# Optimization experiments

Hardware: AMD Instinct MI355X
Metric: run time of the kernel (lower is better)

## Reference

```python
import jax, jax.numpy as jnp
import numpy as np

MAX_DIST = 50.0
NO_NEIGHBORS = 0.0
# feature order: [dx, dy, size_a, size_b, angle]; angle mark is cyclic
FEATURES_RANGE = np.array([50.0, 50.0, 32.0, 32.0, np.pi], dtype=np.float32)
FEATURES_CYCLIC = np.array([False, False, False, False, True])


def setup_inputs() -> dict:
    key = jax.random.key(0)
    ks = jax.random.split(key, 8)
    B, N, M, F, H = 8, 1024, 1024, 5, 4
    points = jax.random.normal(ks[0], (B, N, F), jnp.float32)
    context_points = jax.random.normal(ks[1], (B, M, F), jnp.float32)
    points_mask = jnp.ones((B, N), dtype=bool)
    context_points_mask = jnp.ones((B, M), dtype=bool)
    distance_matrix = jax.random.uniform(ks[2], (B, N, M), jnp.float32) * 100.0
    interactions_mask = jax.random.randint(ks[3], (B, N, M), 0, 2).astype(bool)
    # q_fun MLP: Linear(5,4) -> ReLU -> Linear(4,1) -> Sigmoid
    W1 = jax.random.normal(ks[4], (F, H), jnp.float32) / np.sqrt(F)
    b1 = jnp.zeros((H,), jnp.float32)
    W2 = jax.random.normal(ks[5], (H, 1), jnp.float32) / np.sqrt(H)
    b2 = jnp.zeros((1,), jnp.float32)
    # attention weight model: Linear(5,1)
    Wa = jax.random.normal(ks[6], (F, 1), jnp.float32) / np.sqrt(F)
    ba = jnp.zeros((1,), jnp.float32)
    return dict(points=points, points_mask=points_mask,
                context_points=context_points, context_points_mask=context_points_mask,
                distance_matrix=distance_matrix, interactions_mask=interactions_mask,
                global_max_dist=100,
                W1=W1, b1=b1, W2=W2, b2=b2, Wa=Wa, ba=ba)


def reference(points, points_mask, context_points, context_points_mask,
              distance_matrix, interactions_mask, global_max_dist,
              W1, b1, W2, b2, Wa, ba):
    fr = jnp.asarray(FEATURES_RANGE)
    cyc = jnp.asarray(FEATURES_CYCLIC)
    # pairwise abs feature differences: [B, N, M, 5]
    fd = jnp.abs(points[:, :, None, :] - context_points[:, None, :, :])
    fn = fd / fr
    fc = jnp.remainder(fn, 1.0)
    fc = jnp.minimum(fc, 1.0 - fc)           # cyclic wrap-around distance
    fn = jnp.where(cyc, fc, fn)
    # q_fun MLP + sigmoid -> per-pair similarity energy [B, N, M]
    h = jax.nn.relu(jnp.einsum('bnmf,fh->bnmh', fn, W1) + b1)
    energy = jax.nn.sigmoid(jnp.einsum('bnmh,ho->bnmo', h, W2) + b2)[..., 0]
    # interaction mask, tightened by max_dist when max_dist < global_max_dist
    ib = interactions_mask
    if MAX_DIST < global_max_dist:
        ib = ib & (distance_matrix <= MAX_DIST)
    # masked attention reduce over context axis (dim 2)
    scores = (jnp.einsum('bnmf,fo->bnmo', fn, Wa) + ba)[..., 0]
    scores = jnp.where(ib, scores, -jnp.inf)
    weights = jax.nn.softmax(scores, axis=2)  # all-masked rows -> NaN
    reduced = jnp.sum(weights * energy, axis=2)
    reduced = jnp.nan_to_num(reduced, nan=NO_NEIGHBORS,
                             posinf=NO_NEIGHBORS, neginf=NO_NEIGHBORS)
    return reduced
```

## Files before the change

### kernel.cpp

```cpp
#include <hip/hip_runtime.h>
#include <math.h>

#define BATCH   8
#define NPTS    1024
#define MCTX    1024
#define BN      (BATCH * NPTS)

#define INV_R0  0.02f
#define INV_R1  0.02f
#define INV_R2  0.03125f
#define INV_R3  0.03125f
#define INV_PI  0.3183098861837907f
#define MAX_DIST 50.0f
#define LOG2E   1.4426950408889634f

__global__ __launch_bounds__(512) void sim_kernel(
    const float* __restrict__ points,
    const float* __restrict__ ctx,
    const float* __restrict__ dist,
    const unsigned char* __restrict__ imask,
    const int* __restrict__ gmd_p,
    const float* __restrict__ W1p,
    const float* __restrict__ b1p,
    const float* __restrict__ W2p,
    const float* __restrict__ b2p,
    const float* __restrict__ Wap,
    const float* __restrict__ bap,
    float* __restrict__ out)
{
    __shared__ float4         sA[MCTX];
    __shared__ float          s4[MCTX];
    __shared__ unsigned short q[8][MCTX];

    const int wid  = threadIdx.x >> 6;
    const int lane = threadIdx.x & 63;
    const int row  = blockIdx.x * 8 + wid;
    const int b    = row >> 10;

    const float* __restrict__ cb = ctx + (size_t)b * MCTX * 5;
    const int m0 = threadIdx.x, m1 = threadIdx.x + 512;
    const float r00 = cb[m0*5+0], r01 = cb[m0*5+1], r02 = cb[m0*5+2],
                r03 = cb[m0*5+3], r04 = cb[m0*5+4];
    const float r10 = cb[m1*5+0], r11 = cb[m1*5+1], r12 = cb[m1*5+2],
                r13 = cb[m1*5+3], r14 = cb[m1*5+4];

    const float4*       __restrict__ d4  = (const float4*)(dist + (size_t)row * MCTX);
    const unsigned int* __restrict__ m4p = (const unsigned int*)(imask + (size_t)row * MCTX);
    float4 dv0 = d4[lane],       dv1 = d4[lane + 64],
           dv2 = d4[lane + 128], dv3 = d4[lane + 192];
    unsigned int mv0 = m4p[lane],       mv1 = m4p[lane + 64],
                 mv2 = m4p[lane + 128], mv3 = m4p[lane + 192];

    sA[m0] = make_float4(r00, r01, r02, r03);
    s4[m0] = r04 * INV_PI;
    sA[m1] = make_float4(r10, r11, r12, r13);
    s4[m1] = r14 * INV_PI;
    __syncthreads();

    const float ir[4] = { INV_R0, INV_R1, INV_R2, INV_R3 };
    float w1s[20];
#pragma unroll
    for (int f = 0; f < 5; ++f) {
        const float s = (f < 4) ? ir[f] : 1.0f;
#pragma unroll
        for (int j = 0; j < 4; ++j) w1s[f*4+j] = W1p[f*4+j] * s;
    }
    float b1v[4];
#pragma unroll
    for (int j = 0; j < 4; ++j) b1v[j] = b1p[j];
    float w2n[4];
#pragma unroll
    for (int j = 0; j < 4; ++j) w2n[j] = W2p[j] * (-LOG2E);
    const float b2n = b2p[0] * (-LOG2E);
    float wan[5];
#pragma unroll
    for (int f = 0; f < 5; ++f) wan[f] = Wap[f] * LOG2E * ((f < 4) ? ir[f] : 1.0f);
    const float ban = bap[0] * LOG2E;

    const float p0 = points[row*5+0], p1 = points[row*5+1], p2 = points[row*5+2],
                p3 = points[row*5+3], p4s = points[row*5+4] * INV_PI;

    const bool tighten = (MAX_DIST < (float)gmd_p[0]);

    unsigned okbits = 0;
    {
        const float4 dvv[4] = { dv0, dv1, dv2, dv3 };
        const unsigned int mvv[4] = { mv0, mv1, mv2, mv3 };
#pragma unroll
        for (int j = 0; j < 4; ++j) {
            const float dd[4] = { dvv[j].x, dvv[j].y, dvv[j].z, dvv[j].w };
#pragma unroll
            for (int t = 0; t < 4; ++t) {
                bool ok = ((mvv[j] >> (8*t)) & 0xFFu) != 0u;
                if (tighten) ok = ok && (dd[t] <= MAX_DIST);
                okbits |= ok ? (1u << (4*j + t)) : 0u;
            }
        }
    }

    int tot = 0;
#pragma unroll
    for (int k = 0; k < 16; ++k) {
        const bool ok = (okbits >> k) & 1u;
        unsigned long long bm = __ballot(ok);
        unsigned rank = __builtin_amdgcn_mbcnt_hi(
                            (unsigned)(bm >> 32),
                            __builtin_amdgcn_mbcnt_lo((unsigned)bm, 0u));
        if (ok) {
            const int m = (lane + 64 * (k >> 2)) * 4 + (k & 3);
            q[wid][tot + rank] = (unsigned short)m;
        }
        tot += (int)__popcll(bm);
    }

    float lsum = 0.0f, asum = 0.0f;
#pragma unroll 2
    for (int i = lane; i < tot; i += 64) {
        const int m = (int)q[wid][i];
        const float4 cA  = sA[m];
        const float  c4v = s4[m];

        const float a0 = fabsf(p0 - cA.x);
        const float a1 = fabsf(p1 - cA.y);
        const float a2 = fabsf(p2 - cA.z);
        const float a3 = fabsf(p3 - cA.w);
        float g   = __builtin_amdgcn_fractf(fabsf(p4s - c4v));
        float fn4 = fminf(g, 1.0f - g);

        float h0 = fmaxf(0.0f, b1v[0] + a0*w1s[0] + a1*w1s[4] + a2*w1s[8]  + a3*w1s[12] + fn4*w1s[16]);
        float h1 = fmaxf(0.0f, b1v[1] + a0*w1s[1] + a1*w1s[5] + a2*w1s[9]  + a3*w1s[13] + fn4*w1s[17]);
        float h2 = fmaxf(0.0f, b1v[2] + a0*w1s[2] + a1*w1s[6] + a2*w1s[10] + a3*w1s[14] + fn4*w1s[18]);
        float h3 = fmaxf(0.0f, b1v[3] + a0*w1s[3] + a1*w1s[7] + a2*w1s[11] + a3*w1s[15] + fn4*w1s[19]);

        float zn = b2n + h0*w2n[0] + h1*w2n[1] + h2*w2n[2] + h3*w2n[3];
        float energy = __builtin_amdgcn_rcpf(1.0f + __builtin_amdgcn_exp2f(zn));

        float sc = ban + a0*wan[0] + a1*wan[1] + a2*wan[2] + a3*wan[3] + fn4*wan[4];
        float e  = __builtin_amdgcn_exp2f(sc);

        lsum += e;
        asum = fmaf(e, energy, asum);
    }

#pragma unroll
    for (int off = 1; off < 64; off <<= 1) {
        lsum += __shfl_xor(lsum, off, 64);
        asum += __shfl_xor(asum, off, 64);
    }

    if (lane == 0) {
        out[row] = (lsum > 0.0f) ? (asum / lsum) : 0.0f;
    }
}

extern "C" void kernel_launch(void* const* d_in, const int* in_sizes, int n_in,
                              void* d_out, int out_size, void* d_ws, size_t ws_size,
                              hipStream_t stream) {
    const float*         points = (const float*)d_in[0];
    const float*         ctx    = (const float*)d_in[2];
    const float*         dist   = (const float*)d_in[4];
    const unsigned char* imask  = (const unsigned char*)d_in[5];
    const int*           gmd    = (const int*)d_in[6];
    const float*         W1     = (const float*)d_in[7];
    const float*         b1     = (const float*)d_in[8];
    const float*         W2     = (const float*)d_in[9];
    const float*         b2     = (const float*)d_in[10];
    const float*         Wa     = (const float*)d_in[11];
    const float*         ba     = (const float*)d_in[12];
    float*               out    = (float*)d_out;

    dim3 block(512);
    dim3 grid(BN / 8);
    sim_kernel<<<grid, block, 0, stream>>>(points, ctx, dist, imask, gmd,
                                           W1, b1, W2, b2, Wa, ba, out);
}
```

Measured before the change: 15.47 us.

## Process two rows per wave to amortize context staging across more rows

Each block now handles 16 rows, two per wave, halving the grid so the per-block load of the batch's context points into shared memory and the weight setup are shared by twice as many rows. The second row's distance and mask loads are issued after the barrier so they can overlap with the first row's compaction and compute. The cost is fewer blocks (512 instead of 1024) on a 256-CU device, higher register pressure from holding the second row's loads, and serialized per-wave work. The shared queue is reused across the two rows within each wave.

```diff
diff --git a/kernel.cpp b/kernel.cpp
--- a/kernel.cpp
+++ b/kernel.cpp
@@ -13,6 +13,78 @@
 #define INV_PI  0.3183098861837907f
 #define MAX_DIST 50.0f
 #define LOG2E   1.4426950408889634f
+
+#define PROC_ROW(DV0, DV1, DV2, DV3, MV0, MV1, MV2, MV3, P0, P1, P2, P3, P4S, ROW)   \
+  do {                                                                               \
+    unsigned okbits = 0;                                                             \
+    {                                                                                \
+      const float dd0[4] = { DV0.x, DV0.y, DV0.z, DV0.w };                           \
+      const float dd1[4] = { DV1.x, DV1.y, DV1.z, DV1.w };                           \
+      const float dd2[4] = { DV2.x, DV2.y, DV2.z, DV2.w };                           \
+      const float dd3[4] = { DV3.x, DV3.y, DV3.z, DV3.w };                           \
+      _Pragma("unroll")                                                              \
+      for (int t = 0; t < 4; ++t) {                                                  \
+        bool ok0 = ((MV0 >> (8*t)) & 0xFFu) != 0u;                                   \
+        bool ok1 = ((MV1 >> (8*t)) & 0xFFu) != 0u;                                   \
+        bool ok2 = ((MV2 >> (8*t)) & 0xFFu) != 0u;                                   \
+        bool ok3 = ((MV3 >> (8*t)) & 0xFFu) != 0u;                                   \
+        if (tighten) {                                                               \
+          ok0 = ok0 && (dd0[t] <= MAX_DIST);                                         \
+          ok1 = ok1 && (dd1[t] <= MAX_DIST);                                         \
+          ok2 = ok2 && (dd2[t] <= MAX_DIST);                                         \
+          ok3 = ok3 && (dd3[t] <= MAX_DIST);                                         \
+        }                                                                            \
+        okbits |= ok0 ? (1u << (0  + t)) : 0u;                                       \
+        okbits |= ok1 ? (1u << (4  + t)) : 0u;                                       \
+        okbits |= ok2 ? (1u << (8  + t)) : 0u;                                       \
+        okbits |= ok3 ? (1u << (12 + t)) : 0u;                                       \
+      }                                                                              \
+    }                                                                                \
+    int tot = 0;                                                                     \
+    _Pragma("unroll")                                                                \
+    for (int k = 0; k < 16; ++k) {                                                   \
+      const bool ok = (okbits >> k) & 1u;                                            \
+      unsigned long long bm = __ballot(ok);                                          \
+      unsigned rank = __builtin_amdgcn_mbcnt_hi(                                     \
+                          (unsigned)(bm >> 32),                                      \
+                          __builtin_amdgcn_mbcnt_lo((unsigned)bm, 0u));              \
+      if (ok) {                                                                      \
+        const int m = (lane + 64 * (k >> 2)) * 4 + (k & 3);                          \
+        q[wid][tot + rank] = (unsigned short)m;                                      \
+      }                                                                              \
+      tot += (int)__popcll(bm);                                                      \
+    }                                                                                \
+    float lsum = 0.0f, asum = 0.0f;                                                  \
+    _Pragma("unroll 2")                                                              \
+    for (int i = lane; i < tot; i += 64) {                                           \
+      const int m = (int)q[wid][i];                                                  \
+      const float4 cA  = sA[m];                                                      \
+      const float  c4v = s4[m];                                                      \
+      const float a0 = fabsf(P0 - cA.x);                                             \
+      const float a1 = fabsf(P1 - cA.y);                                             \
+      const float a2 = fabsf(P2 - cA.z);                                             \
+      const float a3 = fabsf(P3 - cA.w);                                             \
+      float g   = __builtin_amdgcn_fractf(fabsf(P4S - c4v));                         \
+      float fn4 = fminf(g, 1.0f - g);                                                \
+      float h0 = fmaxf(0.0f, b1v[0] + a0*w1s[0] + a1*w1s[4] + a2*w1s[8]  + a3*w1s[12] + fn4*w1s[16]); \
+      float h1 = fmaxf(0.0f, b1v[1] + a0*w1s[1] + a1*w1s[5] + a2*w1s[9]  + a3*w1s[13] + fn4*w1s[17]); \
+      float h2 = fmaxf(0.0f, b1v[2] + a0*w1s[2] + a1*w1s[6] + a2*w1s[10] + a3*w1s[14] + fn4*w1s[18]); \
+      float h3 = fmaxf(0.0f, b1v[3] + a0*w1s[3] + a1*w1s[7] + a2*w1s[11] + a3*w1s[15] + fn4*w1s[19]); \
+      float zn = b2n + h0*w2n[0] + h1*w2n[1] + h2*w2n[2] + h3*w2n[3];                \
+      float energy = __builtin_amdgcn_rcpf(1.0f + __builtin_amdgcn_exp2f(zn));       \
+      float sc = ban + a0*wan[0] + a1*wan[1] + a2*wan[2] + a3*wan[3] + fn4*wan[4];   \
+      float e  = __builtin_amdgcn_exp2f(sc);                                         \
+      lsum += e;                                                                     \
+      asum = fmaf(e, energy, asum);                                                  \
+    }                                                                                \
+    _Pragma("unroll")                                                                \
+    for (int off = 1; off < 64; off <<= 1) {                                         \
+      lsum += __shfl_xor(lsum, off, 64);                                             \
+      asum += __shfl_xor(asum, off, 64);                                             \
+    }                                                                                \
+    if (lane == 0)                                                                   \
+      out[ROW] = (lsum > 0.0f) ? (asum / lsum) : 0.0f;                               \
+  } while (0)
 
 __global__ __launch_bounds__(512) void sim_kernel(
     const float* __restrict__ points,
@@ -34,8 +106,10 @@
 
     const int wid  = threadIdx.x >> 6;
     const int lane = threadIdx.x & 63;
-    const int row  = blockIdx.x * 8 + wid;
-    const int b    = row >> 10;
+    const int rb   = blockIdx.x * 16;
+    const int b    = rb >> 10;
+    const int row0 = rb + wid * 2;
+    const int row1 = row0 + 1;
 
     const float* __restrict__ cb = ctx + (size_t)b * MCTX * 5;
     const int m0 = threadIdx.x, m1 = threadIdx.x + 512;
@@ -44,18 +118,25 @@
     const float r10 = cb[m1*5+0], r11 = cb[m1*5+1], r12 = cb[m1*5+2],
                 r13 = cb[m1*5+3], r14 = cb[m1*5+4];
 
-    const float4*       __restrict__ d4  = (const float4*)(dist + (size_t)row * MCTX);
-    const unsigned int* __restrict__ m4p = (const unsigned int*)(imask + (size_t)row * MCTX);
-    float4 dv0 = d4[lane],       dv1 = d4[lane + 64],
-           dv2 = d4[lane + 128], dv3 = d4[lane + 192];
-    unsigned int mv0 = m4p[lane],       mv1 = m4p[lane + 64],
-                 mv2 = m4p[lane + 128], mv3 = m4p[lane + 192];
+    const float4*       __restrict__ dA = (const float4*)(dist + (size_t)row0 * MCTX);
+    const unsigned int* __restrict__ mA = (const unsigned int*)(imask + (size_t)row0 * MCTX);
+    const float4 Adv0 = dA[lane],       Adv1 = dA[lane + 64],
+                 Adv2 = dA[lane + 128], Adv3 = dA[lane + 192];
+    const unsigned int Amv0 = mA[lane],       Amv1 = mA[lane + 64],
+                       Amv2 = mA[lane + 128], Amv3 = mA[lane + 192];
 
     sA[m0] = make_float4(r00, r01, r02, r03);
     s4[m0] = r04 * INV_PI;
     sA[m1] = make_float4(r10, r11, r12, r13);
     s4[m1] = r14 * INV_PI;
     __syncthreads();
+
+    const float4*       __restrict__ dB = (const float4*)(dist + (size_t)row1 * MCTX);
+    const unsigned int* __restrict__ mB = (const unsigned int*)(imask + (size_t)row1 * MCTX);
+    const float4 Bdv0 = dB[lane],       Bdv1 = dB[lane + 64],
+                 Bdv2 = dB[lane + 128], Bdv3 = dB[lane + 192];
+    const unsigned int Bmv0 = mB[lane],       Bmv1 = mB[lane + 64],
+                       Bmv2 = mB[lane + 128], Bmv3 = mB[lane + 192];
 
     const float ir[4] = { INV_R0, INV_R1, INV_R2, INV_R3 };
     float w1s[20];
@@ -77,80 +158,17 @@
     for (int f = 0; f < 5; ++f) wan[f] = Wap[f] * LOG2E * ((f < 4) ? ir[f] : 1.0f);
     const float ban = bap[0] * LOG2E;
 
-    const float p0 = points[row*5+0], p1 = points[row*5+1], p2 = points[row*5+2],
-                p3 = points[row*5+3], p4s = points[row*5+4] * INV_PI;
+    const float p00 = points[row0*5+0], p01 = points[row0*5+1], p02 = points[row0*5+2],
+                p03 = points[row0*5+3], p04s = points[row0*5+4] * INV_PI;
+    const float p10 = points[row1*5+0], p11 = points[row1*5+1], p12 = points[row1*5+2],
+                p13 = points[row1*5+3], p14s = points[row1*5+4] * INV_PI;
 
     const bool tighten = (MAX_DIST < (float)gmd_p[0]);
 
-    unsigned okbits = 0;
-    {
-        const float4 dvv[4] = { dv0, dv1, dv2, dv3 };
-        const unsigned int mvv[4] = { mv0, mv1, mv2, mv3 };
-#pragma unroll
-        for (int j = 0; j < 4; ++j) {
-            const float dd[4] = { dvv[j].x, dvv[j].y, dvv[j].z, dvv[j].w };
-#pragma unroll
-            for (int t = 0; t < 4; ++t) {
-                bool ok = ((mvv[j] >> (8*t)) & 0xFFu) != 0u;
-                if (tighten) ok = ok && (dd[t] <= MAX_DIST);
-                okbits |= ok ? (1u << (4*j + t)) : 0u;
-            }
-        }
-    }
-
-    int tot = 0;
-#pragma unroll
-    for (int k = 0; k < 16; ++k) {
-        const bool ok = (okbits >> k) & 1u;
-        unsigned long long bm = __ballot(ok);
-        unsigned rank = __builtin_amdgcn_mbcnt_hi(
-                            (unsigned)(bm >> 32),
-                            __builtin_amdgcn_mbcnt_lo((unsigned)bm, 0u));
-        if (ok) {
-            const int m = (lane + 64 * (k >> 2)) * 4 + (k & 3);
-            q[wid][tot + rank] = (unsigned short)m;
-        }
-        tot += (int)__popcll(bm);
-    }
-
-    float lsum = 0.0f, asum = 0.0f;
-#pragma unroll 2
-    for (int i = lane; i < tot; i += 64) {
-        const int m = (int)q[wid][i];
-        const float4 cA  = sA[m];
-        const float  c4v = s4[m];
-
-        const float a0 = fabsf(p0 - cA.x);
-        const float a1 = fabsf(p1 - cA.y);
-        const float a2 = fabsf(p2 - cA.z);
-        const float a3 = fabsf(p3 - cA.w);
-        float g   = __builtin_amdgcn_fractf(fabsf(p4s - c4v));
-        float fn4 = fminf(g, 1.0f - g);
-
-        float h0 = fmaxf(0.0f, b1v[0] + a0*w1s[0] + a1*w1s[4] + a2*w1s[8]  + a3*w1s[12] + fn4*w1s[16]);
-        float h1 = fmaxf(0.0f, b1v[1] + a0*w1s[1] + a1*w1s[5] + a2*w1s[9]  + a3*w1s[13] + fn4*w1s[17]);
-        float h2 = fmaxf(0.0f, b1v[2] + a0*w1s[2] + a1*w1s[6] + a2*w1s[10] + a3*w1s[14] + fn4*w1s[18]);
-        float h3 = fmaxf(0.0f, b1v[3] + a0*w1s[3] + a1*w1s[7] + a2*w1s[11] + a3*w1s[15] + fn4*w1s[19]);
-
-        float zn = b2n + h0*w2n[0] + h1*w2n[1] + h2*w2n[2] + h3*w2n[3];
-        float energy = __builtin_amdgcn_rcpf(1.0f + __builtin_amdgcn_exp2f(zn));
-
-        float sc = ban + a0*wan[0] + a1*wan[1] + a2*wan[2] + a3*wan[3] + fn4*wan[4];
-        float e  = __builtin_amdgcn_exp2f(sc);
-
-        lsum += e;
-        asum = fmaf(e, energy, asum);
-    }
-
-#pragma unroll
-    for (int off = 1; off < 64; off <<= 1) {
-        lsum += __shfl_xor(lsum, off, 64);
-        asum += __shfl_xor(asum, off, 64);
-    }
-
-    if (lane == 0) {
-        out[row] = (lsum > 0.0f) ? (asum / lsum) : 0.0f;
-    }
+    PROC_ROW(Adv0, Adv1, Adv2, Adv3, Amv0, Amv1, Amv2, Amv3,
+             p00, p01, p02, p03, p04s, row0);
+    PROC_ROW(Bdv0, Bdv1, Bdv2, Bdv3, Bmv0, Bmv1, Bmv2, Bmv3,
+             p10, p11, p12, p13, p14s, row1);
 }
 
 extern "C" void kernel_launch(void* const* d_in, const int* in_sizes, int n_in,
@@ -170,7 +188,7 @@
     float*               out    = (float*)d_out;
 
     dim3 block(512);
-    dim3 grid(BN / 8);
+    dim3 grid(BN / 16);
     sim_kernel<<<grid, block, 0, stream>>>(points, ctx, dist, imask, gmd,
                                            W1, b1, W2, b2, Wa, ba, out);
 }
```

After: 16.62 us. +7.5%, slower.

## Drop shared-memory context staging; gather context features directly from global memory

Applied to the files above, without the earlier changes.

Removes the per-block cooperative load of all 1024 context points into LDS and the block barrier. The compacted loop now gathers the five context features per pair straight from global memory through the cache, and the row normalisation and log2e scaling move back into the per-pair loop instead of being folded into the weights. Blocks shrink from 8 to 4 waves and the grid doubles, with launch bounds asking for higher occupancy. The trade is uncoalesced 5-float gathers and a few extra multiplies per pair in exchange for less LDS traffic, no barrier, and smaller blocks.

```diff
diff --git a/kernel.cpp b/kernel.cpp
--- a/kernel.cpp
+++ b/kernel.cpp
@@ -14,7 +14,7 @@
 #define MAX_DIST 50.0f
 #define LOG2E   1.4426950408889634f
 
-__global__ __launch_bounds__(512) void sim_kernel(
+__global__ __launch_bounds__(256, 8) void sim_kernel(
     const float* __restrict__ points,
     const float* __restrict__ ctx,
     const float* __restrict__ dist,
@@ -28,58 +28,36 @@
     const float* __restrict__ bap,
     float* __restrict__ out)
 {
-    __shared__ float4         sA[MCTX];
-    __shared__ float          s4[MCTX];
-    __shared__ unsigned short q[8][MCTX];
+    __shared__ unsigned short q[4][MCTX];
 
     const int wid  = threadIdx.x >> 6;
     const int lane = threadIdx.x & 63;
-    const int row  = blockIdx.x * 8 + wid;
+    const int row  = __builtin_amdgcn_readfirstlane((int)blockIdx.x * 4 + wid);
     const int b    = row >> 10;
-
-    const float* __restrict__ cb = ctx + (size_t)b * MCTX * 5;
-    const int m0 = threadIdx.x, m1 = threadIdx.x + 512;
-    const float r00 = cb[m0*5+0], r01 = cb[m0*5+1], r02 = cb[m0*5+2],
-                r03 = cb[m0*5+3], r04 = cb[m0*5+4];
-    const float r10 = cb[m1*5+0], r11 = cb[m1*5+1], r12 = cb[m1*5+2],
-                r13 = cb[m1*5+3], r14 = cb[m1*5+4];
 
     const float4*       __restrict__ d4  = (const float4*)(dist + (size_t)row * MCTX);
     const unsigned int* __restrict__ m4p = (const unsigned int*)(imask + (size_t)row * MCTX);
-    float4 dv0 = d4[lane],       dv1 = d4[lane + 64],
-           dv2 = d4[lane + 128], dv3 = d4[lane + 192];
-    unsigned int mv0 = m4p[lane],       mv1 = m4p[lane + 64],
-                 mv2 = m4p[lane + 128], mv3 = m4p[lane + 192];
+    const float4 dv0 = d4[lane],       dv1 = d4[lane + 64],
+                 dv2 = d4[lane + 128], dv3 = d4[lane + 192];
+    const unsigned int mv0 = m4p[lane],       mv1 = m4p[lane + 64],
+                       mv2 = m4p[lane + 128], mv3 = m4p[lane + 192];
 
-    sA[m0] = make_float4(r00, r01, r02, r03);
-    s4[m0] = r04 * INV_PI;
-    sA[m1] = make_float4(r10, r11, r12, r13);
-    s4[m1] = r14 * INV_PI;
-    __syncthreads();
-
-    const float ir[4] = { INV_R0, INV_R1, INV_R2, INV_R3 };
-    float w1s[20];
+    const float p0 = points[row*5+0], p1 = points[row*5+1], p2 = points[row*5+2],
+                p3 = points[row*5+3], p4 = points[row*5+4];
+    float w1[20];
 #pragma unroll
-    for (int f = 0; f < 5; ++f) {
-        const float s = (f < 4) ? ir[f] : 1.0f;
-#pragma unroll
-        for (int j = 0; j < 4; ++j) w1s[f*4+j] = W1p[f*4+j] * s;
-    }
+    for (int i = 0; i < 20; ++i) w1[i] = W1p[i];
     float b1v[4];
 #pragma unroll
     for (int j = 0; j < 4; ++j) b1v[j] = b1p[j];
-    float w2n[4];
+    float w2[4];
 #pragma unroll
-    for (int j = 0; j < 4; ++j) w2n[j] = W2p[j] * (-LOG2E);
-    const float b2n = b2p[0] * (-LOG2E);
-    float wan[5];
+    for (int j = 0; j < 4; ++j) w2[j] = W2p[j];
+    const float b2v = b2p[0];
+    float wa[5];
 #pragma unroll
-    for (int f = 0; f < 5; ++f) wan[f] = Wap[f] * LOG2E * ((f < 4) ? ir[f] : 1.0f);
-    const float ban = bap[0] * LOG2E;
-
-    const float p0 = points[row*5+0], p1 = points[row*5+1], p2 = points[row*5+2],
-                p3 = points[row*5+3], p4s = points[row*5+4] * INV_PI;
-
+    for (int f = 0; f < 5; ++f) wa[f] = Wap[f];
+    const float bav = bap[0];
     const bool tighten = (MAX_DIST < (float)gmd_p[0]);
 
     unsigned okbits = 0;
@@ -113,30 +91,31 @@
         tot += (int)__popcll(bm);
     }
 
+    const float* __restrict__ cb = ctx + (size_t)b * MCTX * 5;
     float lsum = 0.0f, asum = 0.0f;
 #pragma unroll 2
     for (int i = lane; i < tot; i += 64) {
         const int m = (int)q[wid][i];
-        const float4 cA  = sA[m];
-        const float  c4v = s4[m];
+        const float* __restrict__ c = cb + m * 5;
+        const float c0 = c[0], c1 = c[1], c2 = c[2], c3 = c[3], c4 = c[4];
 
-        const float a0 = fabsf(p0 - cA.x);
-        const float a1 = fabsf(p1 - cA.y);
-        const float a2 = fabsf(p2 - cA.z);
-        const float a3 = fabsf(p3 - cA.w);
-        float g   = __builtin_amdgcn_fractf(fabsf(p4s - c4v));
+        const float a0 = fabsf(p0 - c0) * INV_R0;
+        const float a1 = fabsf(p1 - c1) * INV_R1;
+        const float a2 = fabsf(p2 - c2) * INV_R2;
+        const float a3 = fabsf(p3 - c3) * INV_R3;
+        float g   = __builtin_amdgcn_fractf(fabsf(p4 - c4) * INV_PI);
         float fn4 = fminf(g, 1.0f - g);
 
-        float h0 = fmaxf(0.0f, b1v[0] + a0*w1s[0] + a1*w1s[4] + a2*w1s[8]  + a3*w1s[12] + fn4*w1s[16]);
-        float h1 = fmaxf(0.0f, b1v[1] + a0*w1s[1] + a1*w1s[5] + a2*w1s[9]  + a3*w1s[13] + fn4*w1s[17]);
-        float h2 = fmaxf(0.0f, b1v[2] + a0*w1s[2] + a1*w1s[6] + a2*w1s[10] + a3*w1s[14] + fn4*w1s[18]);
-        float h3 = fmaxf(0.0f, b1v[3] + a0*w1s[3] + a1*w1s[7] + a2*w1s[11] + a3*w1s[15] + fn4*w1s[19]);
+        float h0 = fmaxf(0.0f, b1v[0] + a0*w1[0] + a1*w1[4] + a2*w1[8]  + a3*w1[12] + fn4*w1[16]);
+        float h1 = fmaxf(0.0f, b1v[1] + a0*w1[1] + a1*w1[5] + a2*w1[9]  + a3*w1[13] + fn4*w1[17]);
+        float h2 = fmaxf(0.0f, b1v[2] + a0*w1[2] + a1*w1[6] + a2*w1[10] + a3*w1[14] + fn4*w1[18]);
+        float h3 = fmaxf(0.0f, b1v[3] + a0*w1[3] + a1*w1[7] + a2*w1[11] + a3*w1[15] + fn4*w1[19]);
 
-        float zn = b2n + h0*w2n[0] + h1*w2n[1] + h2*w2n[2] + h3*w2n[3];
-        float energy = __builtin_amdgcn_rcpf(1.0f + __builtin_amdgcn_exp2f(zn));
+        float z  = b2v + h0*w2[0] + h1*w2[1] + h2*w2[2] + h3*w2[3];
+        float energy = __builtin_amdgcn_rcpf(1.0f + __builtin_amdgcn_exp2f(z * (-LOG2E)));
 
-        float sc = ban + a0*wan[0] + a1*wan[1] + a2*wan[2] + a3*wan[3] + fn4*wan[4];
-        float e  = __builtin_amdgcn_exp2f(sc);
+        float score = bav + a0*wa[0] + a1*wa[1] + a2*wa[2] + a3*wa[3] + fn4*wa[4];
+        float e  = __builtin_amdgcn_exp2f(score * LOG2E);
 
         lsum += e;
         asum = fmaf(e, energy, asum);
@@ -169,8 +148,8 @@
     const float*         ba     = (const float*)d_in[12];
     float*               out    = (float*)d_out;
 
-    dim3 block(512);
-    dim3 grid(BN / 8);
+    dim3 block(256);
+    dim3 grid(BN / 4);
     sim_kernel<<<grid, block, 0, stream>>>(points, ctx, dist, imask, gmd,
                                            W1, b1, W2, b2, Wa, ba, out);
 }
```

Result: slower. 16.25 us (+5.1%).
